# Optimization experiments

Measured on AMD Instinct MI355X. Metric: run time of the kernel, lower is better.

Reference implementation:

```python
import jax, jax.numpy as jnp
import numpy as np

B, S, H, I, E = 1, 2048, 2048, 5632, 8
JITTER = 0.01
NEG = jnp.float32(-1e30)  # stands in for -inf; softmax prob underflows to 0


def setup_inputs() -> dict:
    key = jax.random.key(0)
    ks = jax.random.split(key, 5)
    return {
        "hidden_states": jax.random.normal(ks[0], (B, S, H), jnp.float32),
        "gate_w": jax.random.normal(ks[1], (E, H), jnp.float32) * 0.02,   # nn.Linear(H, E) weight
        "w1": jax.random.normal(ks[2], (E, I, H), jnp.float32) * 0.02,    # per-expert w1 weight [out=I, in=H]
        "w2": jax.random.normal(ks[3], (E, H, I), jnp.float32) * 0.02,    # per-expert w2 weight [out=H, in=I]
        "w3": jax.random.normal(ks[4], (E, I, H), jnp.float32) * 0.02,    # per-expert w3 weight [out=I, in=H]
    }


def _sparsemixer_top2(scores, jitter_eps):
    # masked_sampling_omp_inference: sparse-mixer top-2 routing
    top2, sel = jax.lax.top_k(scores, 2)                      # [T,2], [T,2]
    e = scores.shape[-1]
    # --- first expert multiplier ---
    m1 = top2[:, 0:1]                                         # [T,1]
    factor1 = jnp.maximum(jnp.abs(scores), m1)                # clamp(|s|, min=m1)
    mask1 = (m1 - scores) / factor1 > 2.0 * jitter_eps
    p1 = jax.nn.softmax(jnp.where(mask1, NEG, scores), axis=-1)
    mult1 = jnp.take_along_axis(p1, sel[:, 0:1], axis=-1)     # [T,1]
    # --- second expert multiplier (first expert knocked out) ---
    m2 = top2[:, 1:2]
    factor2 = jnp.maximum(jnp.abs(scores), m2)
    mask2 = (m2 - scores) / factor2 > 2.0 * jitter_eps
    onehot0 = sel[:, 0:1] == jnp.arange(e)[None, :]           # scatter(-inf) at top-1 index
    p2 = jax.nn.softmax(jnp.where(onehot0 | mask2, NEG, scores), axis=-1)
    mult2 = jnp.take_along_axis(p2, sel[:, 1:2], axis=-1)     # [T,1]
    return jnp.concatenate([mult1, mult2], axis=-1), sel       # [T,2], [T,2]


def reference(hidden_states, gate_w, w1, w2, w3):
    b, s, h = hidden_states.shape
    x = hidden_states.reshape(-1, h)                          # [T,H]
    logits = x @ gate_w.T                                     # [T,E] router logits
    mult, sel = _sparsemixer_top2(logits, JITTER)
    out = jnp.zeros_like(x)
    for e in range(w1.shape[0]):                              # fixed small expert count
        # combined routing weight for expert e (0 if not selected)
        we = jnp.sum(jnp.where(sel == e, mult, 0.0), axis=-1)  # [T]
        hid = jax.nn.silu(x @ w1[e].T) * (x @ w3[e].T)        # SwiGLU [T,I]
        out = out + we[:, None] * (hid @ w2[e].T)
    return out.reshape(b, s, h)
```

## Files before the change

### kernel.cpp

```cpp
#include <hip/hip_runtime.h>

#define TOKENS 2048
#define HDIM   2048
#define IDIM   5632
#define NEXP   8
#define NSLOT  (TOKENS * 2)
#define BM 128
#define BN 128
#define BK 32

typedef __attribute__((ext_vector_type(8))) short bf16x8;
typedef __attribute__((ext_vector_type(4))) float f32x4;

__device__ __forceinline__ unsigned short f2bf(float f) {
    union { float f; unsigned u; } v; v.f = f;
    unsigned r = v.u + 0x7FFFu + ((v.u >> 16) & 1u);
    return (unsigned short)(r >> 16);
}
__device__ __forceinline__ unsigned pack2(float lo, float hi) {
    return (unsigned)f2bf(lo) | ((unsigned)f2bf(hi) << 16);
}
__device__ __forceinline__ void stage_b_chunk(const float* __restrict__ p, unsigned short* dst) {
    float4 lo = *(const float4*)(p);
    float4 hi = *(const float4*)(p + 4);
    uint4 v;
    v.x = pack2(lo.x, lo.y);
    v.y = pack2(lo.z, lo.w);
    v.z = pack2(hi.x, hi.y);
    v.w = pack2(hi.z, hi.w);
    *(uint4*)dst = v;
}
__device__ __forceinline__ void gl2lds16(const void* g, void* l) {
    __builtin_amdgcn_global_load_lds(
        (const __attribute__((address_space(1))) unsigned int*)g,
        (__attribute__((address_space(3))) unsigned int*)l,
        16, 0, 0);
}

__global__ __launch_bounds__(256) void k_zero(float* __restrict__ out) {
    int i = blockIdx.x * 256 + threadIdx.x;
    float4 z = {0.f, 0.f, 0.f, 0.f};
    ((float4*)out)[i] = z;
}

__global__ __launch_bounds__(256) void k_cvt(const float* __restrict__ src,
                                             unsigned short* __restrict__ dst,
                                             int n8) {
    int stride = gridDim.x * 256;
    for (int i = blockIdx.x * 256 + threadIdx.x; i < n8; i += stride) {
        const float4* p = (const float4*)(src + (size_t)i * 8);
        float4 a = p[0], b = p[1];
        uint4 v;
        v.x = pack2(a.x, a.y); v.y = pack2(a.z, a.w);
        v.z = pack2(b.x, b.y); v.w = pack2(b.z, b.w);
        *(uint4*)(dst + (size_t)i * 8) = v;
    }
}

__global__ __launch_bounds__(256) void k_gate(const float* __restrict__ x,
                                              const float* __restrict__ gw,
                                              int* __restrict__ sel,
                                              float* __restrict__ wts) {
    int wave = threadIdx.x >> 6, lane = threadIdx.x & 63;
    int t = blockIdx.x * 4 + wave;
    const float4* xr = (const float4*)(x + (size_t)t * HDIM);
    const float4* g  = (const float4*)gw;
    float acc[NEXP];
#pragma unroll
    for (int e = 0; e < NEXP; e++) acc[e] = 0.f;
#pragma unroll
    for (int it = 0; it < HDIM / 4 / 64; ++it) {
        int idx = it * 64 + lane;
        float4 xv = xr[idx];
#pragma unroll
        for (int e = 0; e < NEXP; e++) {
            float4 gv = g[e * (HDIM / 4) + idx];
            acc[e] += xv.x * gv.x + xv.y * gv.y + xv.z * gv.z + xv.w * gv.w;
        }
    }
#pragma unroll
    for (int e = 0; e < NEXP; e++) {
        float v = acc[e];
#pragma unroll
        for (int off = 32; off > 0; off >>= 1) v += __shfl_xor(v, off, 64);
        acc[e] = v;
    }
    if (lane == 0) {
        float s[NEXP];
#pragma unroll
        for (int e = 0; e < NEXP; e++) s[e] = acc[e];
        float m1 = s[0]; int i1 = 0;
#pragma unroll
        for (int e = 1; e < NEXP; e++) if (s[e] > m1) { m1 = s[e]; i1 = e; }
        float m2 = -3.0e38f; int i2 = 0;
#pragma unroll
        for (int e = 0; e < NEXP; e++) if (e != i1 && s[e] > m2) { m2 = s[e]; i2 = e; }
        float sum1 = 0.f;
#pragma unroll
        for (int e = 0; e < NEXP; e++) {
            float f = fmaxf(fabsf(s[e]), m1);
            bool masked = ((m1 - s[e]) / f) > 0.02f;
            if (!masked) sum1 += expf(s[e] - m1);
        }
        float sum2 = 0.f;
#pragma unroll
        for (int e = 0; e < NEXP; e++) {
            if (e == i1) continue;
            float f = fmaxf(fabsf(s[e]), m2);
            bool masked = ((m2 - s[e]) / f) > 0.02f;
            if (!masked) sum2 += expf(s[e] - m2);
        }
        sel[2 * t]     = i1;
        sel[2 * t + 1] = i2;
        wts[2 * t]     = 1.f / sum1;
        wts[2 * t + 1] = 1.f / sum2;
    }
}

__global__ __launch_bounds__(256) void k_hist(const int* __restrict__ sel,
                                              int* __restrict__ cnt,
                                              int* __restrict__ offs,
                                              int* __restrict__ cursor) {
    __shared__ int c_s[NEXP];
    int tid = threadIdx.x;
    if (tid < NEXP) c_s[tid] = 0;
    __syncthreads();
    for (int i = tid; i < NSLOT; i += 256) atomicAdd(&c_s[sel[i]], 1);
    __syncthreads();
    if (tid == 0) {
        int o = 0;
        for (int e = 0; e < NEXP; e++) { cnt[e] = c_s[e]; offs[e] = o; o += c_s[e]; cursor[e] = 0; }
    }
}

__global__ __launch_bounds__(256) void k_gather(const float* __restrict__ x,
                                                const int* __restrict__ sel,
                                                const float* __restrict__ wts,
                                                const int* __restrict__ offs,
                                                int* __restrict__ cursor,
                                                int* __restrict__ rowtok,
                                                float* __restrict__ roww,
                                                int* __restrict__ tokslot,
                                                unsigned short* __restrict__ Xe) {
    int t = blockIdx.x;
    __shared__ int slot_s[2];
    if (threadIdx.x == 0) {
        int s0 = sel[2 * t], s1 = sel[2 * t + 1];
        int p0 = offs[s0] + atomicAdd(&cursor[s0], 1);
        int p1 = offs[s1] + atomicAdd(&cursor[s1], 1);
        rowtok[p0] = t; roww[p0] = wts[2 * t];
        rowtok[p1] = t; roww[p1] = wts[2 * t + 1];
        tokslot[2 * t] = p0; tokslot[2 * t + 1] = p1;
        slot_s[0] = p0; slot_s[1] = p1;
    }
    __syncthreads();
    int p0 = slot_s[0], p1 = slot_s[1];
    int base = threadIdx.x * 8;
    const float* xp = x + (size_t)t * HDIM + base;
    float4 a = *(const float4*)(xp);
    float4 b = *(const float4*)(xp + 4);
    uint4 v;
    v.x = pack2(a.x, a.y); v.y = pack2(a.z, a.w);
    v.z = pack2(b.x, b.y); v.w = pack2(b.z, b.w);
    *(uint4*)(Xe + (size_t)p0 * HDIM + base) = v;
    *(uint4*)(Xe + (size_t)p1 * HDIM + base) = v;
}


__global__ __launch_bounds__(256, 2) void k_ffn1_bf(const unsigned short* __restrict__ Xe,
                                                    const unsigned short* __restrict__ w1b,
                                                    const unsigned short* __restrict__ w3b,
                                                    const int* __restrict__ cnt,
                                                    const int* __restrict__ offs,
                                                    unsigned short* __restrict__ hid,
                                                    const float* __restrict__ w2src,
                                                    unsigned short* __restrict__ w2dst) {
    if (blockIdx.z == NEXP) {
        int nblk = gridDim.x * gridDim.y;
        int b = blockIdx.y * gridDim.x + blockIdx.x;
        int n8 = (int)((size_t)NEXP * IDIM * HDIM / 8);
        int stride = nblk * 256;
        for (int i = b * 256 + threadIdx.x; i < n8; i += stride) {
            const float4* p = (const float4*)(w2src + (size_t)i * 8);
            float4 a = p[0], bb = p[1];
            uint4 v;
            v.x = pack2(a.x, a.y);  v.y = pack2(a.z, a.w);
            v.z = pack2(bb.x, bb.y); v.w = pack2(bb.z, bb.w);
            *(uint4*)(w2dst + (size_t)i * 8) = v;
        }
        return;
    }
    int e = blockIdx.z;
    int c = cnt[e];
    int bm = blockIdx.y;
    if (bm * BM >= c) return;
    int n0 = blockIdx.x * BN;
    int row0 = offs[e] + bm * BM;
    int rows_here = c - bm * BM;
    const unsigned short* W1 = w1b + (size_t)e * IDIM * HDIM;
    const unsigned short* W3 = w3b + (size_t)e * IDIM * HDIM;

    __shared__ __align__(16) unsigned short As[16 * 512];
    __shared__ __align__(16) unsigned short B1s[16 * 512];
    __shared__ __align__(16) unsigned short B3s[16 * 512];

    int tid = threadIdx.x, lane = tid & 63, wave = tid >> 6;
    int wm = wave >> 1, wn = wave & 1;
    int fr = lane & 15, kq = lane >> 4;

    f32x4 acc1[4][4], acc3[4][4];
    f32x4 z = {0.f, 0.f, 0.f, 0.f};
#pragma unroll
    for (int i = 0; i < 4; i++)
#pragma unroll
        for (int j = 0; j < 4; j++) { acc1[i][j] = z; acc3[i][j] = z; }

    int ar0 = min(row0 + wave * 16 + fr, NSLOT - 1);
    int ar1 = min(row0 + (wave + 4) * 16 + fr, NSLOT - 1);
    const unsigned short* aP0  = Xe + (size_t)ar0 * HDIM + kq * 8;
    const unsigned short* aP1  = Xe + (size_t)ar1 * HDIM + kq * 8;
    const unsigned short* b1P0 = W1 + (size_t)(n0 + wave * 16 + fr) * HDIM + kq * 8;
    const unsigned short* b1P1 = W1 + (size_t)(n0 + (wave + 4) * 16 + fr) * HDIM + kq * 8;
    const unsigned short* b3P0 = W3 + (size_t)(n0 + wave * 16 + fr) * HDIM + kq * 8;
    const unsigned short* b3P1 = W3 + (size_t)(n0 + (wave + 4) * 16 + fr) * HDIM + kq * 8;

    unsigned short* aL0  = As  + wave * 512;
    unsigned short* aL1  = As  + (wave + 4) * 512;
    unsigned short* b1L0 = B1s + wave * 512;
    unsigned short* b1L1 = B1s + (wave + 4) * 512;
    unsigned short* b3L0 = B3s + wave * 512;
    unsigned short* b3L1 = B3s + (wave + 4) * 512;

    for (int k0 = 0; k0 < HDIM; k0 += 64) {
        __syncthreads();
        gl2lds16(aP0 + k0, aL0);
        gl2lds16(aP1 + k0, aL1);
        gl2lds16(b1P0 + k0, b1L0);
        gl2lds16(b1P1 + k0, b1L1);
        gl2lds16(b3P0 + k0, b3L0);
        gl2lds16(b3P1 + k0, b3L1);
        gl2lds16(aP0 + k0 + 32, aL0 + 4096);
        gl2lds16(aP1 + k0 + 32, aL1 + 4096);
        gl2lds16(b1P0 + k0 + 32, b1L0 + 4096);
        gl2lds16(b1P1 + k0 + 32, b1L1 + 4096);
        gl2lds16(b3P0 + k0 + 32, b3L0 + 4096);
        gl2lds16(b3P1 + k0 + 32, b3L1 + 4096);
        __syncthreads();
#pragma unroll
        for (int h = 0; h < 2; h++) {
            int hb = h * 4096;
            bf16x8 af[4];
#pragma unroll
            for (int i = 0; i < 4; i++)
                af[i] = *(const bf16x8*)&As[hb + ((wm * 4 + i) * 64 + lane) * 8];
#pragma unroll
            for (int j = 0; j < 4; j++) {
                bf16x8 b1f = *(const bf16x8*)&B1s[hb + ((wn * 4 + j) * 64 + lane) * 8];
                bf16x8 b3f = *(const bf16x8*)&B3s[hb + ((wn * 4 + j) * 64 + lane) * 8];
#pragma unroll
                for (int i = 0; i < 4; i++) {
                    acc1[i][j] = __builtin_amdgcn_mfma_f32_16x16x32_bf16(af[i], b1f, acc1[i][j], 0, 0, 0);
                    acc3[i][j] = __builtin_amdgcn_mfma_f32_16x16x32_bf16(af[i], b3f, acc3[i][j], 0, 0, 0);
                }
            }
        }
    }
    int qr = (lane >> 4) * 4, cb = lane & 15;
#pragma unroll
    for (int i = 0; i < 4; i++) {
        int rl = wm * 64 + i * 16 + qr;
#pragma unroll
        for (int v = 0; v < 4; v++) {
            int r = rl + v;
            if (r < rows_here) {
                size_t rowoff = (size_t)(row0 + r) * IDIM;
#pragma unroll
                for (int j = 0; j < 4; j++) {
                    float u1 = acc1[i][j][v], u3 = acc3[i][j][v];
                    float h = u1 * u3 / (1.f + __expf(-u1));
                    hid[rowoff + n0 + wn * 64 + j * 16 + cb] = f2bf(h);
                }
            }
        }
    }
}

__global__ __launch_bounds__(256, 2) void k_ffn2_bf(const unsigned short* __restrict__ hid,
                                                    const unsigned short* __restrict__ w2b,
                                                    const int* __restrict__ cnt,
                                                    const int* __restrict__ offs,
                                                    const float* __restrict__ roww,
                                                    float* __restrict__ Oslot) {
    int e = blockIdx.z;
    int c = cnt[e];
    int bm = blockIdx.y;
    if (bm * BM >= c) return;
    int n0 = blockIdx.x * BN;
    int row0 = offs[e] + bm * BM;
    int rows_here = c - bm * BM;
    const unsigned short* W2 = w2b + (size_t)e * HDIM * IDIM;

    __shared__ __align__(16) unsigned short As[16 * 512];
    __shared__ __align__(16) unsigned short Bs[16 * 512];
    __shared__ float w_s[BM];

    int tid = threadIdx.x, lane = tid & 63, wave = tid >> 6;
    int wm = wave >> 1, wn = wave & 1;
    int fr = lane & 15, kq = lane >> 4;

    if (tid < BM) w_s[tid] = (tid < rows_here) ? roww[row0 + tid] : 0.f;

    f32x4 acc[4][4];
    f32x4 z = {0.f, 0.f, 0.f, 0.f};
#pragma unroll
    for (int i = 0; i < 4; i++)
#pragma unroll
        for (int j = 0; j < 4; j++) acc[i][j] = z;

    int ar0 = min(row0 + wave * 16 + fr, NSLOT - 1);
    int ar1 = min(row0 + (wave + 4) * 16 + fr, NSLOT - 1);
    const unsigned short* aP0 = hid + (size_t)ar0 * IDIM + kq * 8;
    const unsigned short* aP1 = hid + (size_t)ar1 * IDIM + kq * 8;
    const unsigned short* bP0 = W2 + (size_t)(n0 + wave * 16 + fr) * IDIM + kq * 8;
    const unsigned short* bP1 = W2 + (size_t)(n0 + (wave + 4) * 16 + fr) * IDIM + kq * 8;

    unsigned short* aL0 = As + wave * 512;
    unsigned short* aL1 = As + (wave + 4) * 512;
    unsigned short* bL0 = Bs + wave * 512;
    unsigned short* bL1 = Bs + (wave + 4) * 512;

    for (int k0 = 0; k0 < IDIM; k0 += 64) {
        __syncthreads();
        gl2lds16(aP0 + k0, aL0);
        gl2lds16(aP1 + k0, aL1);
        gl2lds16(bP0 + k0, bL0);
        gl2lds16(bP1 + k0, bL1);
        gl2lds16(aP0 + k0 + 32, aL0 + 4096);
        gl2lds16(aP1 + k0 + 32, aL1 + 4096);
        gl2lds16(bP0 + k0 + 32, bL0 + 4096);
        gl2lds16(bP1 + k0 + 32, bL1 + 4096);
        __syncthreads();
#pragma unroll
        for (int h = 0; h < 2; h++) {
            int hb = h * 4096;
            bf16x8 af[4];
#pragma unroll
            for (int i = 0; i < 4; i++)
                af[i] = *(const bf16x8*)&As[hb + ((wm * 4 + i) * 64 + lane) * 8];
#pragma unroll
            for (int j = 0; j < 4; j++) {
                bf16x8 bf = *(const bf16x8*)&Bs[hb + ((wn * 4 + j) * 64 + lane) * 8];
#pragma unroll
                for (int i = 0; i < 4; i++)
                    acc[i][j] = __builtin_amdgcn_mfma_f32_16x16x32_bf16(af[i], bf, acc[i][j], 0, 0, 0);
            }
        }
    }
    int qr = (lane >> 4) * 4, cb = lane & 15;
#pragma unroll
    for (int i = 0; i < 4; i++) {
        int rl = wm * 64 + i * 16 + qr;
#pragma unroll
        for (int v = 0; v < 4; v++) {
            int r = rl + v;
            if (r < rows_here) {
                float wgt = w_s[r];
                float* orow = Oslot + (size_t)(row0 + r) * HDIM + n0 + wn * 64 + cb;
#pragma unroll
                for (int j = 0; j < 4; j++)
                    orow[j * 16] = acc[i][j][v] * wgt;
            }
        }
    }
}

__global__ __launch_bounds__(256) void k_combine(const float* __restrict__ Oslot,
                                                 const int* __restrict__ tokslot,
                                                 float* __restrict__ out) {
    int t = blockIdx.x;
    int p0 = tokslot[2 * t], p1 = tokslot[2 * t + 1];
    int i = threadIdx.x * 8;
    const float4* r0 = (const float4*)(Oslot + (size_t)p0 * HDIM + i);
    const float4* r1 = (const float4*)(Oslot + (size_t)p1 * HDIM + i);
    float4 a0 = r0[0], b0 = r0[1], a1 = r1[0], b1 = r1[1];
    float4 o0 = {a0.x + a1.x, a0.y + a1.y, a0.z + a1.z, a0.w + a1.w};
    float4 o1 = {b0.x + b1.x, b0.y + b1.y, b0.z + b1.z, b0.w + b1.w};
    float* op = out + (size_t)t * HDIM + i;
    *(float4*)op = o0;
    *(float4*)(op + 4) = o1;
}


__global__ __launch_bounds__(256, 2) void k_ffn1_cv(const unsigned short* __restrict__ Xe,
                                                    const float* __restrict__ w1,
                                                    const float* __restrict__ w3,
                                                    const int* __restrict__ cnt,
                                                    const int* __restrict__ offs,
                                                    unsigned short* __restrict__ hid) {
    int e = blockIdx.z;
    int c = cnt[e];
    int bm = blockIdx.y;
    if (bm * BM >= c) return;
    int n0 = blockIdx.x * BN;
    int row0 = offs[e] + bm * BM;
    int rows_here = c - bm * BM;
    const float* W1 = w1 + (size_t)e * IDIM * HDIM;
    const float* W3 = w3 + (size_t)e * IDIM * HDIM;

    __shared__ __align__(16) unsigned short As[8 * 512];
    __shared__ __align__(16) unsigned short B1s[8 * 512];
    __shared__ __align__(16) unsigned short B3s[8 * 512];

    int tid = threadIdx.x, lane = tid & 63, wave = tid >> 6;
    int wm = wave >> 1, wn = wave & 1;
    int fr = lane & 15, kq = lane >> 4;

    f32x4 acc1[4][4], acc3[4][4];
    f32x4 z = {0.f, 0.f, 0.f, 0.f};
#pragma unroll
    for (int i = 0; i < 4; i++)
#pragma unroll
        for (int j = 0; j < 4; j++) { acc1[i][j] = z; acc3[i][j] = z; }

    int ar0 = min(row0 + wave * 16 + fr, NSLOT - 1);
    int ar1 = min(row0 + (wave + 4) * 16 + fr, NSLOT - 1);
    const unsigned short* aP0 = Xe + (size_t)ar0 * HDIM + kq * 8;
    const unsigned short* aP1 = Xe + (size_t)ar1 * HDIM + kq * 8;
    const float* b1P0 = W1 + (size_t)(n0 + wave * 16 + fr) * HDIM + kq * 8;
    const float* b1P1 = W1 + (size_t)(n0 + (wave + 4) * 16 + fr) * HDIM + kq * 8;
    const float* b3P0 = W3 + (size_t)(n0 + wave * 16 + fr) * HDIM + kq * 8;
    const float* b3P1 = W3 + (size_t)(n0 + (wave + 4) * 16 + fr) * HDIM + kq * 8;

    for (int k0 = 0; k0 < HDIM; k0 += BK) {
        __syncthreads();
        *(uint4*)&As[(size_t)tid * 8]         = *(const uint4*)(aP0 + k0);
        *(uint4*)&As[(size_t)(tid + 256) * 8] = *(const uint4*)(aP1 + k0);
        stage_b_chunk(b1P0 + k0, &B1s[(size_t)tid * 8]);
        stage_b_chunk(b1P1 + k0, &B1s[(size_t)(tid + 256) * 8]);
        stage_b_chunk(b3P0 + k0, &B3s[(size_t)tid * 8]);
        stage_b_chunk(b3P1 + k0, &B3s[(size_t)(tid + 256) * 8]);
        __syncthreads();
        bf16x8 af[4];
#pragma unroll
        for (int i = 0; i < 4; i++)
            af[i] = *(const bf16x8*)&As[((wm * 4 + i) * 64 + lane) * 8];
#pragma unroll
        for (int j = 0; j < 4; j++) {
            bf16x8 b1f = *(const bf16x8*)&B1s[((wn * 4 + j) * 64 + lane) * 8];
            bf16x8 b3f = *(const bf16x8*)&B3s[((wn * 4 + j) * 64 + lane) * 8];
#pragma unroll
            for (int i = 0; i < 4; i++) {
                acc1[i][j] = __builtin_amdgcn_mfma_f32_16x16x32_bf16(af[i], b1f, acc1[i][j], 0, 0, 0);
                acc3[i][j] = __builtin_amdgcn_mfma_f32_16x16x32_bf16(af[i], b3f, acc3[i][j], 0, 0, 0);
            }
        }
    }
    int qr = (lane >> 4) * 4, cb = lane & 15;
#pragma unroll
    for (int i = 0; i < 4; i++) {
        int rl = wm * 64 + i * 16 + qr;
#pragma unroll
        for (int v = 0; v < 4; v++) {
            int r = rl + v;
            if (r < rows_here) {
                size_t rowoff = (size_t)(row0 + r) * IDIM;
#pragma unroll
                for (int j = 0; j < 4; j++) {
                    float u1 = acc1[i][j][v], u3 = acc3[i][j][v];
                    float h = u1 * u3 / (1.f + __expf(-u1));
                    hid[rowoff + n0 + wn * 64 + j * 16 + cb] = f2bf(h);
                }
            }
        }
    }
}

__global__ __launch_bounds__(256, 2) void k_ffn2_cv(const unsigned short* __restrict__ hid,
                                                    const float* __restrict__ w2,
                                                    const int* __restrict__ cnt,
                                                    const int* __restrict__ offs,
                                                    const int* __restrict__ rowtok,
                                                    const float* __restrict__ roww,
                                                    float* __restrict__ out) {
    int e = blockIdx.z;
    int c = cnt[e];
    int bm = blockIdx.y;
    if (bm * BM >= c) return;
    int n0 = blockIdx.x * BN;
    int row0 = offs[e] + bm * BM;
    int rows_here = c - bm * BM;
    const float* W2 = w2 + (size_t)e * HDIM * IDIM;

    __shared__ __align__(16) unsigned short As[8 * 512];
    __shared__ __align__(16) unsigned short Bs[8 * 512];
    __shared__ int   tok_s[BM];
    __shared__ float w_s[BM];

    int tid = threadIdx.x, lane = tid & 63, wave = tid >> 6;
    int wm = wave >> 1, wn = wave & 1;
    int fr = lane & 15, kq = lane >> 4;

    if (tid < BM) {
        bool valid = (tid < rows_here);
        tok_s[tid] = valid ? rowtok[row0 + tid] : 0;
        w_s[tid]   = valid ? roww[row0 + tid] : 0.f;
    }

    f32x4 acc[4][4];
    f32x4 z = {0.f, 0.f, 0.f, 0.f};
#pragma unroll
    for (int i = 0; i < 4; i++)
#pragma unroll
        for (int j = 0; j < 4; j++) acc[i][j] = z;

    int ar0 = min(row0 + wave * 16 + fr, NSLOT - 1);
    int ar1 = min(row0 + (wave + 4) * 16 + fr, NSLOT - 1);
    const unsigned short* aP0 = hid + (size_t)ar0 * IDIM + kq * 8;
    const unsigned short* aP1 = hid + (size_t)ar1 * IDIM + kq * 8;
    const float* bP0 = W2 + (size_t)(n0 + wave * 16 + fr) * IDIM + kq * 8;
    const float* bP1 = W2 + (size_t)(n0 + (wave + 4) * 16 + fr) * IDIM + kq * 8;

    for (int k0 = 0; k0 < IDIM; k0 += BK) {
        __syncthreads();
        *(uint4*)&As[(size_t)tid * 8]         = *(const uint4*)(aP0 + k0);
        *(uint4*)&As[(size_t)(tid + 256) * 8] = *(const uint4*)(aP1 + k0);
        stage_b_chunk(bP0 + k0, &Bs[(size_t)tid * 8]);
        stage_b_chunk(bP1 + k0, &Bs[(size_t)(tid + 256) * 8]);
        __syncthreads();
        bf16x8 af[4];
#pragma unroll
        for (int i = 0; i < 4; i++)
            af[i] = *(const bf16x8*)&As[((wm * 4 + i) * 64 + lane) * 8];
#pragma unroll
        for (int j = 0; j < 4; j++) {
            bf16x8 bf = *(const bf16x8*)&Bs[((wn * 4 + j) * 64 + lane) * 8];
#pragma unroll
            for (int i = 0; i < 4; i++)
                acc[i][j] = __builtin_amdgcn_mfma_f32_16x16x32_bf16(af[i], bf, acc[i][j], 0, 0, 0);
        }
    }
    int qr = (lane >> 4) * 4, cb = lane & 15;
#pragma unroll
    for (int i = 0; i < 4; i++) {
        int rl = wm * 64 + i * 16 + qr;
#pragma unroll
        for (int v = 0; v < 4; v++) {
            int r = rl + v;
            if (r < rows_here) {
                int tok = tok_s[r];
                float wgt = w_s[r];
                float* orow = out + (size_t)tok * HDIM + n0 + wn * 64 + cb;
#pragma unroll
                for (int j = 0; j < 4; j++)
                    atomicAdd(orow + j * 16, acc[i][j][v] * wgt);
            }
        }
    }
}

extern "C" void kernel_launch(void* const* d_in, const int* in_sizes, int n_in,
                              void* d_out, int out_size, void* d_ws, size_t ws_size,
                              hipStream_t stream) {
    const float* x  = (const float*)d_in[0];
    const float* gw = (const float*)d_in[1];
    const float* w1 = (const float*)d_in[2];
    const float* w2 = (const float*)d_in[3];
    const float* w3 = (const float*)d_in[4];
    float* out = (float*)d_out;

    char* ws = (char*)d_ws;
    int*   sel     = (int*)(ws);
    float* wts     = (float*)(ws + 16 * 1024);
    int*   cnt     = (int*)(ws + 32 * 1024);
    int*   offs    = (int*)(ws + 32 * 1024 + 256);
    int*   cursor  = (int*)(ws + 32 * 1024 + 512);
    int*   rowtok  = (int*)(ws + 48 * 1024);
    float* roww    = (float*)(ws + 64 * 1024);
    int*   tokslot = (int*)(ws + 80 * 1024);
    unsigned short* Xe  = (unsigned short*)(ws + (1ull << 20));
    unsigned short* hid = (unsigned short*)(ws + (18ull << 20));
    float*          Osl = (float*)(ws + (64ull << 20));
    unsigned short* w1b = (unsigned short*)(ws + (100ull << 20));
    unsigned short* w3b = (unsigned short*)(ws + (290ull << 20));
    unsigned short* w2sep = (unsigned short*)(ws + (480ull << 20));

    const size_t EIH  = (size_t)NEXP * IDIM * HDIM;
    const size_t REQ1 = (290ull << 20) + EIH * 2;
    const size_t REQ2 = (480ull << 20) + EIH * 2;

    k_gate<<<dim3(TOKENS / 4), dim3(256), 0, stream>>>(x, gw, sel, wts);
    k_hist<<<dim3(1), dim3(256), 0, stream>>>(sel, cnt, offs, cursor);
    k_gather<<<dim3(TOKENS), dim3(256), 0, stream>>>(x, sel, wts, offs, cursor, rowtok, roww, tokslot, Xe);

    if (ws_size >= REQ1) {
        bool sep = (ws_size >= REQ2);
        unsigned short* w2b = sep ? w2sep : w1b;

        k_cvt<<<dim3(2048), dim3(256), 0, stream>>>(w1, w1b, (int)(EIH / 8));
        k_cvt<<<dim3(2048), dim3(256), 0, stream>>>(w3, w3b, (int)(EIH / 8));
        if (sep) {
            k_ffn1_bf<<<dim3(IDIM / BN, TOKENS / BM, NEXP + 1), dim3(256), 0, stream>>>(
                Xe, w1b, w3b, cnt, offs, hid, w2, w2b);
        } else {
            k_ffn1_bf<<<dim3(IDIM / BN, TOKENS / BM, NEXP), dim3(256), 0, stream>>>(
                Xe, w1b, w3b, cnt, offs, hid, nullptr, nullptr);
            k_cvt<<<dim3(2048), dim3(256), 0, stream>>>(w2, w2b, (int)(EIH / 8));
        }
        k_ffn2_bf<<<dim3(HDIM / BN, TOKENS / BM, NEXP), dim3(256), 0, stream>>>(hid, w2b, cnt, offs, roww, Osl);
        k_combine<<<dim3(TOKENS), dim3(256), 0, stream>>>(Osl, tokslot, out);
    } else {
        k_zero<<<dim3((TOKENS * HDIM / 4) / 256), dim3(256), 0, stream>>>(out);
        k_ffn1_cv<<<dim3(IDIM / BN, TOKENS / BM, NEXP), dim3(256), 0, stream>>>(Xe, w1, w3, cnt, offs, hid);
        k_ffn2_cv<<<dim3(HDIM / BN, TOKENS / BM, NEXP), dim3(256), 0, stream>>>(hid, w2, cnt, offs, rowtok, roww, out);
    }
}
```

Baseline: 1.797 ms.

## Double-buffer LDS staging in FFN GEMMs and use hardware bf16 pack

Replaces the load-then-compute loop in both expert GEMM kernels with a two-buffer ping-pong. The next BK=32 slice is issued via global_load_lds while the current slice feeds the MFMAs, so global latency can overlap with compute. LDS footprint per block stays the same because the two halves of the old 64-wide tile become the two buffers. It also swaps the manual float-to-bf16 rounding in pack2 for the HIP __float22bfloat162_rn intrinsic. There is a correctness risk: the async LDS loads may not be waited on before the barrier, since nothing explicitly waits on vmcnt.

```diff
diff --git a/kernel.cpp b/kernel.cpp
--- a/kernel.cpp
+++ b/kernel.cpp
@@ -1,4 +1,5 @@
 #include <hip/hip_runtime.h>
+#include <hip/hip_bf16.h>
 
 #define TOKENS 2048
 #define HDIM   2048
@@ -18,7 +19,10 @@
     return (unsigned short)(r >> 16);
 }
 __device__ __forceinline__ unsigned pack2(float lo, float hi) {
-    return (unsigned)f2bf(lo) | ((unsigned)f2bf(hi) << 16);
+    float2 f; f.x = lo; f.y = hi;
+    __hip_bfloat162 h = __float22bfloat162_rn(f);
+    union { __hip_bfloat162 h; unsigned u; } c; c.h = h;
+    return c.u;
 }
 __device__ __forceinline__ void stage_b_chunk(const float* __restrict__ p, unsigned short* dst) {
     float4 lo = *(const float4*)(p);
@@ -167,6 +171,34 @@
 }
 
 
+#define FFN1_STAGE(b, k)                                           \
+    do {                                                           \
+        gl2lds16(aP0 + (k),  As  + (b) * 4096 + wave * 512);       \
+        gl2lds16(aP1 + (k),  As  + (b) * 4096 + (wave + 4) * 512); \
+        gl2lds16(b1P0 + (k), B1s + (b) * 4096 + wave * 512);       \
+        gl2lds16(b1P1 + (k), B1s + (b) * 4096 + (wave + 4) * 512); \
+        gl2lds16(b3P0 + (k), B3s + (b) * 4096 + wave * 512);       \
+        gl2lds16(b3P1 + (k), B3s + (b) * 4096 + (wave + 4) * 512); \
+    } while (0)
+
+#define FFN1_COMPUTE(b)                                                                       \
+    do {                                                                                      \
+        bf16x8 af[4];                                                                         \
+        _Pragma("unroll")                                                                     \
+        for (int i = 0; i < 4; i++)                                                           \
+            af[i] = *(const bf16x8*)&As[(b) * 4096 + ((wm * 4 + i) * 64 + lane) * 8];         \
+        _Pragma("unroll")                                                                     \
+        for (int j = 0; j < 4; j++) {                                                         \
+            bf16x8 b1f = *(const bf16x8*)&B1s[(b) * 4096 + ((wn * 4 + j) * 64 + lane) * 8];   \
+            bf16x8 b3f = *(const bf16x8*)&B3s[(b) * 4096 + ((wn * 4 + j) * 64 + lane) * 8];   \
+            _Pragma("unroll")                                                                 \
+            for (int i = 0; i < 4; i++) {                                                     \
+                acc1[i][j] = __builtin_amdgcn_mfma_f32_16x16x32_bf16(af[i], b1f, acc1[i][j], 0, 0, 0); \
+                acc3[i][j] = __builtin_amdgcn_mfma_f32_16x16x32_bf16(af[i], b3f, acc3[i][j], 0, 0, 0); \
+            }                                                                                 \
+        }                                                                                     \
+    } while (0)
+
 __global__ __launch_bounds__(256, 2) void k_ffn1_bf(const unsigned short* __restrict__ Xe,
                                                     const unsigned short* __restrict__ w1b,
                                                     const unsigned short* __restrict__ w3b,
@@ -184,7 +216,7 @@
             const float4* p = (const float4*)(w2src + (size_t)i * 8);
             float4 a = p[0], bb = p[1];
             uint4 v;
-            v.x = pack2(a.x, a.y);  v.y = pack2(a.z, a.w);
+            v.x = pack2(a.x, a.y);   v.y = pack2(a.z, a.w);
             v.z = pack2(bb.x, bb.y); v.w = pack2(bb.z, bb.w);
             *(uint4*)(w2dst + (size_t)i * 8) = v;
         }
@@ -200,9 +232,9 @@
     const unsigned short* W1 = w1b + (size_t)e * IDIM * HDIM;
     const unsigned short* W3 = w3b + (size_t)e * IDIM * HDIM;
 
-    __shared__ __align__(16) unsigned short As[16 * 512];
-    __shared__ __align__(16) unsigned short B1s[16 * 512];
-    __shared__ __align__(16) unsigned short B3s[16 * 512];
+    __shared__ __align__(16) unsigned short As[2 * 4096];
+    __shared__ __align__(16) unsigned short B1s[2 * 4096];
+    __shared__ __align__(16) unsigned short B3s[2 * 4096];
 
     int tid = threadIdx.x, lane = tid & 63, wave = tid >> 6;
     int wm = wave >> 1, wn = wave & 1;
@@ -224,46 +256,15 @@
     const unsigned short* b3P0 = W3 + (size_t)(n0 + wave * 16 + fr) * HDIM + kq * 8;
     const unsigned short* b3P1 = W3 + (size_t)(n0 + (wave + 4) * 16 + fr) * HDIM + kq * 8;
 
-    unsigned short* aL0  = As  + wave * 512;
-    unsigned short* aL1  = As  + (wave + 4) * 512;
-    unsigned short* b1L0 = B1s + wave * 512;
-    unsigned short* b1L1 = B1s + (wave + 4) * 512;
-    unsigned short* b3L0 = B3s + wave * 512;
-    unsigned short* b3L1 = B3s + (wave + 4) * 512;
-
-    for (int k0 = 0; k0 < HDIM; k0 += 64) {
-        __syncthreads();
-        gl2lds16(aP0 + k0, aL0);
-        gl2lds16(aP1 + k0, aL1);
-        gl2lds16(b1P0 + k0, b1L0);
-        gl2lds16(b1P1 + k0, b1L1);
-        gl2lds16(b3P0 + k0, b3L0);
-        gl2lds16(b3P1 + k0, b3L1);
-        gl2lds16(aP0 + k0 + 32, aL0 + 4096);
-        gl2lds16(aP1 + k0 + 32, aL1 + 4096);
-        gl2lds16(b1P0 + k0 + 32, b1L0 + 4096);
-        gl2lds16(b1P1 + k0 + 32, b1L1 + 4096);
-        gl2lds16(b3P0 + k0 + 32, b3L0 + 4096);
-        gl2lds16(b3P1 + k0 + 32, b3L1 + 4096);
-        __syncthreads();
-#pragma unroll
-        for (int h = 0; h < 2; h++) {
-            int hb = h * 4096;
-            bf16x8 af[4];
-#pragma unroll
-            for (int i = 0; i < 4; i++)
-                af[i] = *(const bf16x8*)&As[hb + ((wm * 4 + i) * 64 + lane) * 8];
-#pragma unroll
-            for (int j = 0; j < 4; j++) {
-                bf16x8 b1f = *(const bf16x8*)&B1s[hb + ((wn * 4 + j) * 64 + lane) * 8];
-                bf16x8 b3f = *(const bf16x8*)&B3s[hb + ((wn * 4 + j) * 64 + lane) * 8];
-#pragma unroll
-                for (int i = 0; i < 4; i++) {
-                    acc1[i][j] = __builtin_amdgcn_mfma_f32_16x16x32_bf16(af[i], b1f, acc1[i][j], 0, 0, 0);
-                    acc3[i][j] = __builtin_amdgcn_mfma_f32_16x16x32_bf16(af[i], b3f, acc3[i][j], 0, 0, 0);
-                }
-            }
-        }
+    FFN1_STAGE(0, 0);
+    __syncthreads();
+    for (int k0 = 0; k0 < HDIM; k0 += 2 * BK) {
+        if (k0 + BK < HDIM) FFN1_STAGE(1, k0 + BK);
+        FFN1_COMPUTE(0);
+        __syncthreads();
+        if (k0 + 2 * BK < HDIM) FFN1_STAGE(0, k0 + 2 * BK);
+        FFN1_COMPUTE(1);
+        __syncthreads();
     }
     int qr = (lane >> 4) * 4, cb = lane & 15;
 #pragma unroll
@@ -284,6 +285,29 @@
         }
     }
 }
+
+#define FFN2_STAGE(b, k)                                          \
+    do {                                                          \
+        gl2lds16(aP0 + (k), As + (b) * 4096 + wave * 512);        \
+        gl2lds16(aP1 + (k), As + (b) * 4096 + (wave + 4) * 512);  \
+        gl2lds16(bP0 + (k), Bs + (b) * 4096 + wave * 512);        \
+        gl2lds16(bP1 + (k), Bs + (b) * 4096 + (wave + 4) * 512);  \
+    } while (0)
+
+#define FFN2_COMPUTE(b)                                                                     \
+    do {                                                                                    \
+        bf16x8 af[4];                                                                       \
+        _Pragma("unroll")                                                                   \
+        for (int i = 0; i < 4; i++)                                                         \
+            af[i] = *(const bf16x8*)&As[(b) * 4096 + ((wm * 4 + i) * 64 + lane) * 8];       \
+        _Pragma("unroll")                                                                   \
+        for (int j = 0; j < 4; j++) {                                                       \
+            bf16x8 bf = *(const bf16x8*)&Bs[(b) * 4096 + ((wn * 4 + j) * 64 + lane) * 8];   \
+            _Pragma("unroll")                                                               \
+            for (int i = 0; i < 4; i++)                                                     \
+                acc[i][j] = __builtin_amdgcn_mfma_f32_16x16x32_bf16(af[i], bf, acc[i][j], 0, 0, 0); \
+        }                                                                                   \
+    } while (0)
 
 __global__ __launch_bounds__(256, 2) void k_ffn2_bf(const unsigned short* __restrict__ hid,
                                                     const unsigned short* __restrict__ w2b,
@@ -300,8 +324,8 @@
     int rows_here = c - bm * BM;
     const unsigned short* W2 = w2b + (size_t)e * HDIM * IDIM;
 
-    __shared__ __align__(16) unsigned short As[16 * 512];
-    __shared__ __align__(16) unsigned short Bs[16 * 512];
+    __shared__ __align__(16) unsigned short As[2 * 4096];
+    __shared__ __align__(16) unsigned short Bs[2 * 4096];
     __shared__ float w_s[BM];
 
     int tid = threadIdx.x, lane = tid & 63, wave = tid >> 6;
@@ -324,37 +348,15 @@
     const unsigned short* bP0 = W2 + (size_t)(n0 + wave * 16 + fr) * IDIM + kq * 8;
     const unsigned short* bP1 = W2 + (size_t)(n0 + (wave + 4) * 16 + fr) * IDIM + kq * 8;
 
-    unsigned short* aL0 = As + wave * 512;
-    unsigned short* aL1 = As + (wave + 4) * 512;
-    unsigned short* bL0 = Bs + wave * 512;
-    unsigned short* bL1 = Bs + (wave + 4) * 512;
-
-    for (int k0 = 0; k0 < IDIM; k0 += 64) {
-        __syncthreads();
-        gl2lds16(aP0 + k0, aL0);
-        gl2lds16(aP1 + k0, aL1);
-        gl2lds16(bP0 + k0, bL0);
-        gl2lds16(bP1 + k0, bL1);
-        gl2lds16(aP0 + k0 + 32, aL0 + 4096);
-        gl2lds16(aP1 + k0 + 32, aL1 + 4096);
-        gl2lds16(bP0 + k0 + 32, bL0 + 4096);
-        gl2lds16(bP1 + k0 + 32, bL1 + 4096);
-        __syncthreads();
-#pragma unroll
-        for (int h = 0; h < 2; h++) {
-            int hb = h * 4096;
-            bf16x8 af[4];
-#pragma unroll
-            for (int i = 0; i < 4; i++)
-                af[i] = *(const bf16x8*)&As[hb + ((wm * 4 + i) * 64 + lane) * 8];
-#pragma unroll
-            for (int j = 0; j < 4; j++) {
-                bf16x8 bf = *(const bf16x8*)&Bs[hb + ((wn * 4 + j) * 64 + lane) * 8];
-#pragma unroll
-                for (int i = 0; i < 4; i++)
-                    acc[i][j] = __builtin_amdgcn_mfma_f32_16x16x32_bf16(af[i], bf, acc[i][j], 0, 0, 0);
-            }
-        }
+    FFN2_STAGE(0, 0);
+    __syncthreads();
+    for (int k0 = 0; k0 < IDIM; k0 += 2 * BK) {
+        if (k0 + BK < IDIM) FFN2_STAGE(1, k0 + BK);
+        FFN2_COMPUTE(0);
+        __syncthreads();
+        if (k0 + 2 * BK < IDIM) FFN2_STAGE(0, k0 + 2 * BK);
+        FFN2_COMPUTE(1);
+        __syncthreads();
     }
     int qr = (lane >> 4) * 4, cb = lane & 15;
 #pragma unroll
```

Measured after the change: 1.766 ms. Within noise of the previous version (-1.7%).
